# Kernel optimization log

Measured on AMD Instinct MI355X. Metric: run time of the kernel, lower is better.

Reference implementation:

```python
import jax, jax.numpy as jnp
import numpy as np

NEG_SLOPE = 0.01  # nn.LeakyReLU default


def setup_inputs() -> dict:
    key = jax.random.key(0)
    k1, k2, k3, k4, k5, k6 = jax.random.split(key, 6)
    N, E, F_IN, F_OUT = 50000, 800000, 256, 64
    x = jax.random.normal(k1, (N, F_IN), dtype=jnp.float32)
    src = jax.random.randint(k2, (E,), 0, N, dtype=jnp.int32)
    dst = jax.random.randint(k3, (E,), 0, N, dtype=jnp.int32)
    # nn.init.normal_(weight, 0, 0.5) for both Linear layers (no bias)
    W1 = 0.5 * jax.random.normal(k4, (F_OUT, F_IN), dtype=jnp.float32)
    W2 = 0.5 * jax.random.normal(k5, (F_OUT, F_OUT), dtype=jnp.float32)
    # detGAT.a = torch.rand(2*out_feats, 1)
    a = jax.random.uniform(k6, (2 * F_OUT, 1), dtype=jnp.float32)
    return {"x": x, "W1": W1, "W2": W2, "a": a, "src": src, "dst": dst}


def reference(x, W1, W2, a, src, dst):
    N, d = x.shape[0], W1.shape[0]
    # model_base: linear -> (dropout, identity in eval) -> relu, twice
    z = jax.nn.relu(x @ W1.T)
    h = jax.nn.relu(z @ W2.T)  # [N, d]
    # detGAT edge score: LeakyReLU(concat([h_dst, h_src]) @ a)
    # split a so we compute per-node dot products once instead of an [E, 2d] concat
    a_dst, a_src = a[:d, 0], a[d:, 0]
    s_dst = h @ a_dst  # [N]
    s_src = h @ a_src  # [N]
    score = jax.nn.leaky_relu(s_dst[dst] + s_src[src], NEG_SLOPE)  # [E]
    # edge_softmax: softmax over incoming edges of each destination node
    m = jax.ops.segment_max(score, dst, num_segments=N)  # [N]
    e = jnp.exp(score - m[dst])
    ssum = jax.ops.segment_sum(e, dst, num_segments=N)  # [N]
    w = e / ssum[dst]  # [E]
    # weighted scatter-sum of src features to dst nodes
    res = jax.ops.segment_sum(h[src] * w[:, None], dst, num_segments=N)  # [N, d]
    return jax.nn.relu(h - res)
```

## Files before the change

### kernel.cpp

```cpp
#include <hip/hip_runtime.h>
#include <math.h>

#define F_IN 256
#define F_OUT 64
#define NEG_SLOPE 0.01f
#define CAP 8192
#define NB2 256

typedef unsigned short ushort8_t __attribute__((ext_vector_type(8)));
typedef __bf16 bf16x8 __attribute__((ext_vector_type(8)));
typedef float f32x16 __attribute__((ext_vector_type(16)));

__device__ inline unsigned short f2bf(float f) {
    unsigned u = __float_as_uint(f);
    u += 0x7FFF + ((u >> 16) & 1);
    return (unsigned short)(u >> 16);
}
__device__ inline float bf2f(unsigned short u) {
    return __uint_as_float(((unsigned)u) << 16);
}
__device__ inline void splitbf(float x, unsigned short& hi, unsigned short& lo) {
    hi = f2bf(x);
    lo = f2bf(x - bf2f(hi));
}
__device__ inline bf16x8 asbf8(ushort8_t u) {
    union { ushort8_t u; bf16x8 b; } c; c.u = u; return c.b;
}

__global__ __launch_bounds__(256)
void prep_frag_kernel(const float* __restrict__ W1, const float* __restrict__ W2,
                      unsigned short* __restrict__ w1fh, unsigned short* __restrict__ w1fl,
                      unsigned short* __restrict__ w2fh, unsigned short* __restrict__ w2fl)
{
    int idx = blockIdx.x * blockDim.x + threadIdx.x;
    int jj = idx & 7, l = (idx >> 3) & 63, t = idx >> 9;
    {
        int nt = t & 1, gks = t >> 1;
        int f = nt * 32 + (l & 31);
        int k = gks * 16 + (l >> 5) * 8 + jj;
        unsigned short hi, lo;
        splitbf(W1[f * F_IN + k], hi, lo);
        w1fh[idx] = hi; w1fl[idx] = lo;
    }
    if (idx < 4096) {
        int nt = t & 1, ks = t >> 1;
        int f = nt * 32 + (l & 31);
        int j = ks * 16 + (l >> 5) * 8 + jj;
        unsigned short hi, lo;
        splitbf(W2[f * F_OUT + j], hi, lo);
        w2fh[idx] = hi; w2fl[idx] = lo;
    }
}

__global__ __launch_bounds__(256, 4)
void mlp_kernel(const float* __restrict__ x,
                const unsigned short* __restrict__ w1fh,
                const unsigned short* __restrict__ w1fl,
                const unsigned short* __restrict__ w2fh,
                const unsigned short* __restrict__ w2fl,
                const float* __restrict__ a,
                unsigned short* __restrict__ hb,
                float* __restrict__ sdst,
                float* __restrict__ ssrc, int N)
{
    __shared__ __align__(16) char smem[34304];
    __shared__ float sred[8][64];
    unsigned short* xh  = (unsigned short*)smem;
    unsigned short* xl  = (unsigned short*)(smem + 17152);
    unsigned short* zh16 = (unsigned short*)smem;
    unsigned short* zl16 = (unsigned short*)(smem + 8448);
    float* zhf = (float*)(smem + 17408);

    const int tid = threadIdx.x;
    const int lane = tid & 63;
    const int wq = __builtin_amdgcn_readfirstlane(tid >> 6);
    const int mt = wq >> 1, nt = wq & 1;
    const int ml = lane & 31;
    const int q = lane >> 5;
    const int node0 = blockIdx.x * 64;

    const int r = tid >> 2, g = tid & 3;
    const int gnode = min(node0 + r, N - 1);
    const float* __restrict__ xsrc = x + (size_t)gnode * F_IN + g * 32;

    f32x16 acc;
#pragma unroll
    for (int i = 0; i < 16; i++) acc[i] = 0.f;

    float4 v[8];
#pragma unroll
    for (int i = 0; i < 8; i++) v[i] = *(const float4*)(xsrc + i * 4);

#pragma unroll
    for (int half = 0; half < 2; half++) {
        __syncthreads();
#pragma unroll
        for (int i = 0; i < 8; i++) {
            int kidx = r * 134 + g * 32 + i * 4;
            ushort4 hi4, lo4;
            splitbf(v[i].x, hi4.x, lo4.x);
            splitbf(v[i].y, hi4.y, lo4.y);
            splitbf(v[i].z, hi4.z, lo4.z);
            splitbf(v[i].w, hi4.w, lo4.w);
            *(ushort4*)(xh + kidx) = hi4;
            *(ushort4*)(xl + kidx) = lo4;
        }
        __syncthreads();
        if (half == 0) {
#pragma unroll
            for (int i = 0; i < 8; i++)
                v[i] = *(const float4*)(xsrc + 128 + i * 4);
        }
#pragma unroll
        for (int ks = 0; ks < 8; ks++) {
            int gks = half * 8 + ks;
            bf16x8 bh = asbf8(*(const ushort8_t*)(w1fh + (((gks * 2 + nt) * 64) + lane) * 8));
            bf16x8 bl = asbf8(*(const ushort8_t*)(w1fl + (((gks * 2 + nt) * 64) + lane) * 8));
            int aidx = (mt * 32 + ml) * 134 + ks * 16 + q * 8;
            bf16x8 ah = asbf8(*(const ushort8_t*)(xh + aidx));
            bf16x8 al = asbf8(*(const ushort8_t*)(xl + aidx));
            acc = __builtin_amdgcn_mfma_f32_32x32x16_bf16(ah, bh, acc, 0, 0, 0);
            acc = __builtin_amdgcn_mfma_f32_32x32x16_bf16(ah, bl, acc, 0, 0, 0);
            acc = __builtin_amdgcn_mfma_f32_32x32x16_bf16(al, bh, acc, 0, 0, 0);
        }
    }
    __syncthreads();

#pragma unroll
    for (int reg = 0; reg < 16; reg++) {
        int nd = mt * 32 + (reg & 3) + 8 * (reg >> 2) + 4 * q;
        float z = fmaxf(acc[reg], 0.f);
        unsigned short hi, lo;
        splitbf(z, hi, lo);
        zh16[nd * 66 + nt * 32 + ml] = hi;
        zl16[nd * 66 + nt * 32 + ml] = lo;
    }
    __syncthreads();

    f32x16 hacc;
#pragma unroll
    for (int i = 0; i < 16; i++) hacc[i] = 0.f;
#pragma unroll
    for (int ks = 0; ks < 4; ks++) {
        bf16x8 bh = asbf8(*(const ushort8_t*)(w2fh + (((ks * 2 + nt) * 64) + lane) * 8));
        bf16x8 bl = asbf8(*(const ushort8_t*)(w2fl + (((ks * 2 + nt) * 64) + lane) * 8));
        int aidx = (mt * 32 + ml) * 66 + ks * 16 + q * 8;
        bf16x8 ah = asbf8(*(const ushort8_t*)(zh16 + aidx));
        bf16x8 al = asbf8(*(const ushort8_t*)(zl16 + aidx));
        hacc = __builtin_amdgcn_mfma_f32_32x32x16_bf16(ah, bh, hacc, 0, 0, 0);
        hacc = __builtin_amdgcn_mfma_f32_32x32x16_bf16(ah, bl, hacc, 0, 0, 0);
        hacc = __builtin_amdgcn_mfma_f32_32x32x16_bf16(al, bh, hacc, 0, 0, 0);
    }
#pragma unroll
    for (int reg = 0; reg < 16; reg++) {
        int nd = mt * 32 + (reg & 3) + 8 * (reg >> 2) + 4 * q;
        zhf[nd * 65 + nt * 32 + ml] = fmaxf(hacc[reg], 0.f);
    }
    __syncthreads();

    float sd = 0.f, ss = 0.f;
#pragma unroll
    for (int f = 0; f < 16; f++) {
        float hf = zhf[lane * 65 + wq * 16 + f];
        sd = fmaf(hf, a[wq * 16 + f], sd);
        ss = fmaf(hf, a[F_OUT + wq * 16 + f], ss);
    }
    sred[wq][lane] = sd;
    sred[4 + wq][lane] = ss;
    __syncthreads();

    if (tid < 64) {
        int node = node0 + lane;
        if (node < N) {
            sdst[node] = sred[0][lane] + sred[1][lane] + sred[2][lane] + sred[3][lane];
            ssrc[node] = sred[4][lane] + sred[5][lane] + sred[6][lane] + sred[7][lane];
        }
    }
#pragma unroll
    for (int i = 0; i < 2; i++) {
        int idx = tid + 256 * i;
        int nn = idx >> 3;
        int c0 = (idx & 7) * 8;
        if (node0 + nn < N) {
            ushort8_t vv;
#pragma unroll
            for (int c = 0; c < 8; c++) vv[c] = f2bf(zhf[nn * 65 + c0 + c]);
            *(ushort8_t*)(hb + (size_t)(node0 + nn) * F_OUT + c0) = vv;
        }
    }
}

__global__ __launch_bounds__(1024)
void scatter_fused_kernel(const int* __restrict__ src, const int* __restrict__ dst,
                          int* __restrict__ cursor, int* __restrict__ edata,
                          int E, int chunk)
{
    __shared__ int lh[256], lbase[256], lcur[256];
    const int tid = threadIdx.x;
    if (tid < 256) lh[tid] = 0;
    __syncthreads();
    const int beg = blockIdx.x * chunk;
    const int end = min(E, beg + chunk);
    for (int i = beg + tid; i < end; i += 1024)
        atomicAdd(&lh[((unsigned)dst[i]) >> 8], 1);
    __syncthreads();
    if (tid < 256) {
        int c = lh[tid];
        lbase[tid] = c ? atomicAdd(&cursor[tid], c) : 0;
        lcur[tid] = 0;
    }
    __syncthreads();
    for (int i = beg + tid; i < end; i += 1024) {
        int d = dst[i];
        int s = src[i];
        int b = ((unsigned)d) >> 8;
        int rk = atomicAdd(&lcur[b], 1);
        edata[b * CAP + lbase[b] + rk] = ((d & 0xFF) << 16) | s;
    }
}

__global__ __launch_bounds__(1024)
void bucket_sort_kernel(const int* __restrict__ cursor,
                        const int* __restrict__ edata,
                        int* __restrict__ ssorted,
                        int* __restrict__ cnt, int* __restrict__ offs, int N)
{
    __shared__ int hist[256];
    __shared__ int excl[256];
    const int tid = threadIdx.x;
    const int lane = tid & 63;
    const int cb = blockIdx.x;
    const int base = cb * CAP;
    const int ecnt = cursor[cb];

    if (tid < 256) hist[tid] = 0;
    __syncthreads();
    for (int i = tid; i < ecnt; i += 1024)
        atomicAdd(&hist[((unsigned)edata[base + i]) >> 16], 1);
    __syncthreads();

    if (tid < 64) {
        int v0 = hist[lane * 4], v1 = hist[lane * 4 + 1];
        int v2 = hist[lane * 4 + 2], v3 = hist[lane * 4 + 3];
        int ts = v0 + v1 + v2 + v3;
        int s = ts;
#pragma unroll
        for (int d = 1; d < 64; d <<= 1) {
            int t = __shfl_up(s, d);
            if (lane >= d) s += t;
        }
        int e = s - ts;
        excl[lane * 4] = e;
        excl[lane * 4 + 1] = e + v0;
        excl[lane * 4 + 2] = e + v0 + v1;
        excl[lane * 4 + 3] = e + v0 + v1 + v2;
    }
    __syncthreads();

    if (tid < 256) {
        int d = cb * 256 + tid;
        if (d < N) {
            cnt[d] = hist[tid];
            offs[d] = base + excl[tid];
        }
    }
    __syncthreads();

    for (int i = tid; i < ecnt; i += 1024) {
        int pack = edata[base + i];
        int low = ((unsigned)pack) >> 16;
        int rk = atomicAdd(&excl[low], 1);
        ssorted[base + rk] = pack & 0xFFFF;
    }
}

__global__ __launch_bounds__(256)
void aggregate_kernel(const unsigned short* __restrict__ hb,
                      const float* __restrict__ sdst,
                      const float* __restrict__ ssrc,
                      const int* __restrict__ offs,
                      const int* __restrict__ cnt,
                      const int* __restrict__ ssorted,
                      float* __restrict__ out, int N)
{
    __shared__ float2 ws_sh[4][64];
    const int lane = threadIdx.x & 63;
    const int wid = threadIdx.x >> 6;
    const int d = blockIdx.x * 4 + wid;
    if (d >= N) return;

    const int off = offs[d];
    const int deg = cnt[d];
    const float sdd = sdst[d];
    float M = -INFINITY, S = 0.f, res = 0.f;

    for (int cb = 0; cb < deg; cb += 64) {
        int ce = min(64, deg - cb);
        float score = -INFINITY;
        int s = 0;
        if (lane < ce) {
            s = ssorted[off + cb + lane];
            float sc = sdd + ssrc[s];
            score = sc > 0.f ? sc : NEG_SLOPE * sc;
        }
        float mc = score;
#pragma unroll
        for (int dd = 32; dd > 0; dd >>= 1)
            mc = fmaxf(mc, __shfl_xor(mc, dd));
        float newM = fmaxf(M, mc);
        float scale = __expf(M - newM);
        float w = (lane < ce) ? __expf(score - newM) : 0.f;
        ws_sh[wid][lane] = make_float2(w, __int_as_float(s));
        float csum = w;
#pragma unroll
        for (int dd = 32; dd > 0; dd >>= 1)
            csum += __shfl_xor(csum, dd);
        S = S * scale + csum;
        __builtin_amdgcn_wave_barrier();

        float c[8];
#pragma unroll
        for (int i = 0; i < 8; i++) c[i] = 0.f;
        const int ceo = (ce + 7) & ~7;
        for (int e = 0; e < ceo; e += 8) {
#pragma unroll
            for (int i = 0; i < 8; i++) {
                float2 t = ws_sh[wid][e + i];
                int se = __builtin_amdgcn_readfirstlane(__float_as_int(t.y));
                c[i] = fmaf(t.x, bf2f(hb[((unsigned)se << 6) + lane]), c[i]);
            }
        }
        float t = ((c[0] + c[1]) + (c[2] + c[3])) + ((c[4] + c[5]) + (c[6] + c[7]));
        res = res * scale + t;
        __builtin_amdgcn_wave_barrier();
        M = newM;
    }

    float hf = bf2f(hb[((unsigned)d << 6) + lane]);
    float r = (S > 0.f) ? (hf - res / S) : hf;
    out[(size_t)d * F_OUT + lane] = r > 0.f ? r : 0.f;
}

extern "C" void kernel_launch(void* const* d_in, const int* in_sizes, int n_in,
                              void* d_out, int out_size, void* d_ws,
                              size_t ws_size, hipStream_t stream)
{
    const float* x  = (const float*)d_in[0];
    const float* W1 = (const float*)d_in[1];
    const float* W2 = (const float*)d_in[2];
    const float* a  = (const float*)d_in[3];
    const int* src  = (const int*)d_in[4];
    const int* dst  = (const int*)d_in[5];
    const int N = in_sizes[0] / F_IN;
    const int E = in_sizes[4];

    float* ws = (float*)d_ws;
    float* sdst = ws;
    float* ssrc = sdst + N;
    unsigned short* w1fh = (unsigned short*)(ssrc + N);
    unsigned short* w1fl = w1fh + 16384;
    unsigned short* w2fh = w1fl + 16384;
    unsigned short* w2fl = w2fh + 4096;
    unsigned short* hb = w2fl + 4096;
    int* cnt    = (int*)(hb + (size_t)N * F_OUT);
    int* offs   = cnt + N;
    int* cursor = offs + N;
    int* edata  = cursor + 256;
    int* ssorted = edata + 196 * CAP;

    const int nbc = (N + 255) >> 8;
    const int chunk = (E + NB2 - 1) / NB2;

    hipMemsetAsync(cursor, 0, 256 * sizeof(int), stream);
    prep_frag_kernel<<<64, 256, 0, stream>>>(W1, W2, w1fh, w1fl, w2fh, w2fl);
    mlp_kernel<<<(N + 63) / 64, 256, 0, stream>>>(x, w1fh, w1fl, w2fh, w2fl, a,
                                                  hb, sdst, ssrc, N);
    scatter_fused_kernel<<<NB2, 1024, 0, stream>>>(src, dst, cursor, edata, E, chunk);
    bucket_sort_kernel<<<nbc, 1024, 0, stream>>>(cursor, edata, ssorted, cnt, offs, N);
    aggregate_kernel<<<(N + 3) / 4, 256, 0, stream>>>(hb, sdst, ssrc, offs, cnt,
                                                      ssorted, (float*)d_out, N);
}
```

Measured before the change: 176.3 us.

## Restructure MLP kernel to per-wave 32-row tiles loading x directly into registers

```diff
diff --git a/kernel.cpp b/kernel.cpp
--- a/kernel.cpp
+++ b/kernel.cpp
@@ -25,6 +25,24 @@
 }
 __device__ inline bf16x8 asbf8(ushort8_t u) {
     union { ushort8_t u; bf16x8 b; } c; c.u = u; return c.b;
+}
+__device__ inline void split8(const float4& p0, const float4& p1, bf16x8& ah, bf16x8& al) {
+    ushort8_t h, l;
+    unsigned short th, tl;
+    splitbf(p0.x, th, tl); h[0] = th; l[0] = tl;
+    splitbf(p0.y, th, tl); h[1] = th; l[1] = tl;
+    splitbf(p0.z, th, tl); h[2] = th; l[2] = tl;
+    splitbf(p0.w, th, tl); h[3] = th; l[3] = tl;
+    splitbf(p1.x, th, tl); h[4] = th; l[4] = tl;
+    splitbf(p1.y, th, tl); h[5] = th; l[5] = tl;
+    splitbf(p1.z, th, tl); h[6] = th; l[6] = tl;
+    splitbf(p1.w, th, tl); h[7] = th; l[7] = tl;
+    ah = asbf8(h); al = asbf8(l);
+}
+__device__ inline float redq32(float v) {
+    v += __shfl_xor(v, 1);  v += __shfl_xor(v, 2);  v += __shfl_xor(v, 4);
+    v += __shfl_xor(v, 8);  v += __shfl_xor(v, 16);
+    return v;
 }
 
 __global__ __launch_bounds__(256)
@@ -52,7 +70,7 @@
     }
 }
 
-__global__ __launch_bounds__(256, 4)
+__global__ __launch_bounds__(128, 2)
 void mlp_kernel(const float* __restrict__ x,
                 const unsigned short* __restrict__ w1fh,
                 const unsigned short* __restrict__ w1fl,
@@ -63,129 +81,109 @@
                 float* __restrict__ sdst,
                 float* __restrict__ ssrc, int N)
 {
-    __shared__ __align__(16) char smem[34304];
-    __shared__ float sred[8][64];
-    unsigned short* xh  = (unsigned short*)smem;
-    unsigned short* xl  = (unsigned short*)(smem + 17152);
-    unsigned short* zh16 = (unsigned short*)smem;
-    unsigned short* zl16 = (unsigned short*)(smem + 8448);
-    float* zhf = (float*)(smem + 17408);
+    __shared__ __align__(16) unsigned short zbuf[2 * 4224];
 
     const int tid = threadIdx.x;
     const int lane = tid & 63;
-    const int wq = __builtin_amdgcn_readfirstlane(tid >> 6);
-    const int mt = wq >> 1, nt = wq & 1;
+    const int w = __builtin_amdgcn_readfirstlane(tid >> 6);
     const int ml = lane & 31;
     const int q = lane >> 5;
-    const int node0 = blockIdx.x * 64;
-
-    const int r = tid >> 2, g = tid & 3;
-    const int gnode = min(node0 + r, N - 1);
-    const float* __restrict__ xsrc = x + (size_t)gnode * F_IN + g * 32;
-
-    f32x16 acc;
-#pragma unroll
-    for (int i = 0; i < 16; i++) acc[i] = 0.f;
-
-    float4 v[8];
-#pragma unroll
-    for (int i = 0; i < 8; i++) v[i] = *(const float4*)(xsrc + i * 4);
-
-#pragma unroll
-    for (int half = 0; half < 2; half++) {
-        __syncthreads();
-#pragma unroll
-        for (int i = 0; i < 8; i++) {
-            int kidx = r * 134 + g * 32 + i * 4;
-            ushort4 hi4, lo4;
-            splitbf(v[i].x, hi4.x, lo4.x);
-            splitbf(v[i].y, hi4.y, lo4.y);
-            splitbf(v[i].z, hi4.z, lo4.z);
-            splitbf(v[i].w, hi4.w, lo4.w);
-            *(ushort4*)(xh + kidx) = hi4;
-            *(ushort4*)(xl + kidx) = lo4;
-        }
-        __syncthreads();
-        if (half == 0) {
-#pragma unroll
-            for (int i = 0; i < 8; i++)
-                v[i] = *(const float4*)(xsrc + 128 + i * 4);
-        }
-#pragma unroll
-        for (int ks = 0; ks < 8; ks++) {
-            int gks = half * 8 + ks;
-            bf16x8 bh = asbf8(*(const ushort8_t*)(w1fh + (((gks * 2 + nt) * 64) + lane) * 8));
-            bf16x8 bl = asbf8(*(const ushort8_t*)(w1fl + (((gks * 2 + nt) * 64) + lane) * 8));
-            int aidx = (mt * 32 + ml) * 134 + ks * 16 + q * 8;
-            bf16x8 ah = asbf8(*(const ushort8_t*)(xh + aidx));
-            bf16x8 al = asbf8(*(const ushort8_t*)(xl + aidx));
-            acc = __builtin_amdgcn_mfma_f32_32x32x16_bf16(ah, bh, acc, 0, 0, 0);
-            acc = __builtin_amdgcn_mfma_f32_32x32x16_bf16(ah, bl, acc, 0, 0, 0);
-            acc = __builtin_amdgcn_mfma_f32_32x32x16_bf16(al, bh, acc, 0, 0, 0);
-        }
-    }
-    __syncthreads();
+    const int node0w = blockIdx.x * 64 + w * 32;
+
+    unsigned short* zh = zbuf + w * 4224;
+    unsigned short* zl = zh + 2112;
+
+    const int rowc = min(node0w + ml, N - 1);
+    const float* __restrict__ xrow = x + (size_t)rowc * F_IN + q * 8;
+
+    f32x16 acc0, acc1;
+#pragma unroll
+    for (int i = 0; i < 16; i++) { acc0[i] = 0.f; acc1[i] = 0.f; }
+
+    float4 p0 = *(const float4*)(xrow);
+    float4 p1 = *(const float4*)(xrow + 4);
+    ushort8_t b0h = *(const ushort8_t*)(w1fh + (lane) * 8);
+    ushort8_t b0l = *(const ushort8_t*)(w1fl + (lane) * 8);
+    ushort8_t b1h = *(const ushort8_t*)(w1fh + (64 + lane) * 8);
+    ushort8_t b1l = *(const ushort8_t*)(w1fl + (64 + lane) * 8);
+
+#pragma unroll
+    for (int gks = 0; gks < 16; gks++) {
+        const int nx = gks < 15 ? gks + 1 : 15;
+        float4 q0 = *(const float4*)(xrow + nx * 16);
+        float4 q1 = *(const float4*)(xrow + nx * 16 + 4);
+        ushort8_t c0h = *(const ushort8_t*)(w1fh + ((nx * 2 + 0) * 64 + lane) * 8);
+        ushort8_t c0l = *(const ushort8_t*)(w1fl + ((nx * 2 + 0) * 64 + lane) * 8);
+        ushort8_t c1h = *(const ushort8_t*)(w1fh + ((nx * 2 + 1) * 64 + lane) * 8);
+        ushort8_t c1l = *(const ushort8_t*)(w1fl + ((nx * 2 + 1) * 64 + lane) * 8);
+
+        bf16x8 ah, al;
+        split8(p0, p1, ah, al);
+        acc0 = __builtin_amdgcn_mfma_f32_32x32x16_bf16(ah, asbf8(b0h), acc0, 0, 0, 0);
+        acc0 = __builtin_amdgcn_mfma_f32_32x32x16_bf16(ah, asbf8(b0l), acc0, 0, 0, 0);
+        acc0 = __builtin_amdgcn_mfma_f32_32x32x16_bf16(al, asbf8(b0h), acc0, 0, 0, 0);
+        acc1 = __builtin_amdgcn_mfma_f32_32x32x16_bf16(ah, asbf8(b1h), acc1, 0, 0, 0);
+        acc1 = __builtin_amdgcn_mfma_f32_32x32x16_bf16(ah, asbf8(b1l), acc1, 0, 0, 0);
+        acc1 = __builtin_amdgcn_mfma_f32_32x32x16_bf16(al, asbf8(b1h), acc1, 0, 0, 0);
+
+        p0 = q0; p1 = q1;
+        b0h = c0h; b0l = c0l; b1h = c1h; b1l = c1l;
+    }
 
 #pragma unroll
     for (int reg = 0; reg < 16; reg++) {
-        int nd = mt * 32 + (reg & 3) + 8 * (reg >> 2) + 4 * q;
-        float z = fmaxf(acc[reg], 0.f);
-        unsigned short hi, lo;
-        splitbf(z, hi, lo);
-        zh16[nd * 66 + nt * 32 + ml] = hi;
-        zl16[nd * 66 + nt * 32 + ml] = lo;
-    }
-    __syncthreads();
-
-    f32x16 hacc;
-#pragma unroll
-    for (int i = 0; i < 16; i++) hacc[i] = 0.f;
+        int nd = (reg & 3) + 8 * (reg >> 2) + 4 * q;
+        float z0 = fmaxf(acc0[reg], 0.f);
+        float z1 = fmaxf(acc1[reg], 0.f);
+        unsigned short h_, l_;
+        splitbf(z0, h_, l_);
+        zh[nd * 66 + ml] = h_; zl[nd * 66 + ml] = l_;
+        splitbf(z1, h_, l_);
+        zh[nd * 66 + 32 + ml] = h_; zl[nd * 66 + 32 + ml] = l_;
+    }
+
+    f32x16 hacc0, hacc1;
+#pragma unroll
+    for (int i = 0; i < 16; i++) { hacc0[i] = 0.f; hacc1[i] = 0.f; }
 #pragma unroll
     for (int ks = 0; ks < 4; ks++) {
-        bf16x8 bh = asbf8(*(const ushort8_t*)(w2fh + (((ks * 2 + nt) * 64) + lane) * 8));
-        bf16x8 bl = asbf8(*(const ushort8_t*)(w2fl + (((ks * 2 + nt) * 64) + lane) * 8));
-        int aidx = (mt * 32 + ml) * 66 + ks * 16 + q * 8;
-        bf16x8 ah = asbf8(*(const ushort8_t*)(zh16 + aidx));
-        bf16x8 al = asbf8(*(const ushort8_t*)(zl16 + aidx));
-        hacc = __builtin_amdgcn_mfma_f32_32x32x16_bf16(ah, bh, hacc, 0, 0, 0);
-        hacc = __builtin_amdgcn_mfma_f32_32x32x16_bf16(ah, bl, hacc, 0, 0, 0);
-        hacc = __builtin_amdgcn_mfma_f32_32x32x16_bf16(al, bh, hacc, 0, 0, 0);
-    }
+        ushort8_t wh0 = *(const ushort8_t*)(w2fh + ((ks * 2 + 0) * 64 + lane) * 8);
+        ushort8_t wl0 = *(const ushort8_t*)(w2fl + ((ks * 2 + 0) * 64 + lane) * 8);
+        ushort8_t wh1 = *(const ushort8_t*)(w2fh + ((ks * 2 + 1) * 64 + lane) * 8);
+        ushort8_t wl1 = *(const ushort8_t*)(w2fl + ((ks * 2 + 1) * 64 + lane) * 8);
+        bf16x8 ah = asbf8(*(const ushort8_t*)(zh + ml * 66 + ks * 16 + q * 8));
+        bf16x8 al = asbf8(*(const ushort8_t*)(zl + ml * 66 + ks * 16 + q * 8));
+        hacc0 = __builtin_amdgcn_mfma_f32_32x32x16_bf16(ah, asbf8(wh0), hacc0, 0, 0, 0);
+        hacc0 = __builtin_amdgcn_mfma_f32_32x32x16_bf16(ah, asbf8(wl0), hacc0, 0, 0, 0);
+        hacc0 = __builtin_amdgcn_mfma_f32_32x32x16_bf16(al, asbf8(wh0), hacc0, 0, 0, 0);
+        hacc1 = __builtin_amdgcn_mfma_f32_32x32x16_bf16(ah, asbf8(wh1), hacc1, 0, 0, 0);
+        hacc1 = __builtin_amdgcn_mfma_f32_32x32x16_bf16(ah, asbf8(wl1), hacc1, 0, 0, 0);
+        hacc1 = __builtin_amdgcn_mfma_f32_32x32x16_bf16(al, asbf8(wh1), hacc1, 0, 0, 0);
+    }
+
+    const float aD0 = a[ml],            aD1 = a[32 + ml];
+    const float aS0 = a[F_OUT + ml],    aS1 = a[F_OUT + 32 + ml];
+
+    float sdv = 0.f, ssv = 0.f;
 #pragma unroll
     for (int reg = 0; reg < 16; reg++) {
-        int nd = mt * 32 + (reg & 3) + 8 * (reg >> 2) + 4 * q;
-        zhf[nd * 65 + nt * 32 + ml] = fmaxf(hacc[reg], 0.f);
-    }
-    __syncthreads();
-
-    float sd = 0.f, ss = 0.f;
-#pragma unroll
-    for (int f = 0; f < 16; f++) {
-        float hf = zhf[lane * 65 + wq * 16 + f];
-        sd = fmaf(hf, a[wq * 16 + f], sd);
-        ss = fmaf(hf, a[F_OUT + wq * 16 + f], ss);
-    }
-    sred[wq][lane] = sd;
-    sred[4 + wq][lane] = ss;
-    __syncthreads();
-
-    if (tid < 64) {
-        int node = node0 + lane;
-        if (node < N) {
-            sdst[node] = sred[0][lane] + sred[1][lane] + sred[2][lane] + sred[3][lane];
-            ssrc[node] = sred[4][lane] + sred[5][lane] + sred[6][lane] + sred[7][lane];
-        }
-    }
-#pragma unroll
-    for (int i = 0; i < 2; i++) {
-        int idx = tid + 256 * i;
-        int nn = idx >> 3;
-        int c0 = (idx & 7) * 8;
-        if (node0 + nn < N) {
-            ushort8_t vv;
-#pragma unroll
-            for (int c = 0; c < 8; c++) vv[c] = f2bf(zhf[nn * 65 + c0 + c]);
-            *(ushort8_t*)(hb + (size_t)(node0 + nn) * F_OUT + c0) = vv;
+        int nd = (reg & 3) + 8 * (reg >> 2) + 4 * q;
+        float h0 = fmaxf(hacc0[reg], 0.f);
+        float h1 = fmaxf(hacc1[reg], 0.f);
+        float td = redq32(h0 * aD0 + h1 * aD1);
+        float ts = redq32(h0 * aS0 + h1 * aS1);
+        if (ml == nd) { sdv = td; ssv = ts; }
+        int gn = node0w + nd;
+        if (gn < N) {
+            hb[(size_t)gn * F_OUT + ml]      = f2bf(h0);
+            hb[(size_t)gn * F_OUT + 32 + ml] = f2bf(h1);
+        }
+    }
+    {
+        int gn = node0w + ml;
+        if ((((ml >> 2) & 1) == q) && gn < N) {
+            sdst[gn] = sdv;
+            ssrc[gn] = ssv;
         }
     }
 }
@@ -373,7 +371,7 @@
 
     hipMemsetAsync(cursor, 0, 256 * sizeof(int), stream);
     prep_frag_kernel<<<64, 256, 0, stream>>>(W1, W2, w1fh, w1fl, w2fh, w2fl);
-    mlp_kernel<<<(N + 63) / 64, 256, 0, stream>>>(x, w1fh, w1fl, w2fh, w2fl, a,
+    mlp_kernel<<<(N + 63) / 64, 128, 0, stream>>>(x, w1fh, w1fl, w2fh, w2fl, a,
                                                   hb, sdst, ssrc, N);
     scatter_fused_kernel<<<NB2, 1024, 0, stream>>>(src, dst, cursor, edata, E, chunk);
     bucket_sort_kernel<<<nbc, 1024, 0, stream>>>(cursor, edata, ssorted, cnt, offs, N);
```

Measured after the change: 164.3 us. 6.8% less time.
